# Optimization experiments

Measured on AMD Instinct MI355X. Metric: run time of the kernel, lower is better.

Reference implementation:

```python
import jax, jax.numpy as jnp
import numpy as np

B, T, D, H = 64, 512, 512, 1024


def setup_inputs() -> dict:
    key = jax.random.key(0)
    k1, k2, k3 = jax.random.split(key, 3)
    x = jax.random.normal(k1, (B, T, D), dtype=jnp.float32)
    W = jax.random.normal(k2, (D, 4 * H), dtype=jnp.float32) * 0.02  # input kernel
    U = jax.random.normal(k3, (H, 4 * H), dtype=jnp.float32) * 0.02  # recurrent kernel
    b = jnp.zeros((4 * H,), dtype=jnp.float32)
    return {"x": x, "W": W, "U": U, "b": b}


def reference(x, W, U, b):
    # Keras LSTM, gate order [i, f, c(g), o], sigmoid recurrent activation, tanh activation.
    # return_sequences=False, return_state=True -> pred == h_T; output = concat([h_T, h_T, c_T]).
    batch = x.shape[0]
    hidden = U.shape[0]

    def step(carry, xt):
        h, c = carry
        z = xt @ W + h @ U + b  # [B, 4H]
        i, f, g, o = jnp.split(z, 4, axis=-1)
        i = jax.nn.sigmoid(i)
        f = jax.nn.sigmoid(f)
        o = jax.nn.sigmoid(o)
        c_new = f * c + i * jnp.tanh(g)
        h_new = o * jnp.tanh(c_new)
        return (h_new, c_new), None

    h0 = jnp.zeros((batch, hidden), dtype=x.dtype)
    c0 = jnp.zeros((batch, hidden), dtype=x.dtype)
    xs = jnp.swapaxes(x, 0, 1)  # [T, B, D]
    (hT, cT), _ = jax.lax.scan(step, (h0, c0), xs)
    return jnp.concatenate([hT, hT, cT], axis=-1)  # [B, 3H]
```

## Files before the change

kernel.cpp:

```cpp
#include <hip/hip_runtime.h>
#include <stdint.h>

typedef unsigned short u16;

#define T_STEPS 512
#define BATCH   64
#define DIN     512
#define HID     1024
#define G4      4096
#define NBLK    128
#define NH      8
#define NC      32
#define THREADS 512

#define U_LD    1032
#define W_LD    520

#define SM_BYTES 99328
#define WT_OFF   66048

#define XB_BYTES ((size_t)T_STEPS * BATCH * DIN * 2)
#define HB_OFF   XB_BYTES
#define HB_BYTES (2u * 2u * 128 * 32 * 8 * 2)
#define FLG_OFF  (HB_OFF + HB_BYTES)
#define FLG_BYTES (2 * 128 * 4 * 16)
#define WS_NEED  (FLG_OFF + FLG_BYTES)

typedef float f32x16 __attribute__((ext_vector_type(16)));
typedef short bf16x8 __attribute__((ext_vector_type(8)));
typedef unsigned uint32x4 __attribute__((ext_vector_type(4)));

__device__ __forceinline__ u16 f2bf(float f) {
  unsigned u = __float_as_uint(f);
  u += 0x7fffu + ((u >> 16) & 1u);
  return (u16)(u >> 16);
}
__device__ __forceinline__ float sigm(float x) {
  return __builtin_amdgcn_rcpf(1.f + __expf(-x));
}
__device__ __forceinline__ float fast_tanh(float x) {
  return 1.f - 2.f * __builtin_amdgcn_rcpf(__expf(2.f * x) + 1.f);
}

__device__ __forceinline__ uint32x4 load16_sc(uint64_t addr) {
  uint32x4 d;
  asm volatile("global_load_dwordx4 %0, %1, off sc0 sc1" : "=v"(d) : "v"(addr));
  return d;
}
__device__ __forceinline__ uint32x4 load16_plain(uint64_t addr) {
  uint32x4 d;
  asm volatile("global_load_dwordx4 %0, %1, off" : "=v"(d) : "v"(addr));
  return d;
}
__device__ __forceinline__ unsigned load4_sc(uint64_t addr) {
  unsigned d;
  asm volatile("global_load_dword %0, %1, off sc0 sc1" : "=v"(d) : "v"(addr));
  return d;
}
__device__ __forceinline__ void store16_sc(uint64_t addr, uint32x4 v) {
  asm volatile("global_store_dwordx4 %0, %1, off sc0 sc1" :: "v"(addr), "v"(v) : "memory");
}
__device__ __forceinline__ void store4_sc(uint64_t addr, unsigned v) {
  asm volatile("global_store_dword %0, %1, off sc0 sc1" :: "v"(addr), "v"(v) : "memory");
}
#define WAITV(n) asm volatile("s_waitcnt vmcnt(" #n ")" ::: "memory")
#define SBAR()   __builtin_amdgcn_sched_barrier(0)

__global__ void cvt_x(const float* __restrict__ x, u16* __restrict__ xb) {
  int i = blockIdx.x * 256 + threadIdx.x;
  int dblk = i & 63;
  int rest = i >> 6;
  int b = rest & 63;
  int t = rest >> 6;
  const float4* s = reinterpret_cast<const float4*>(x + ((size_t)(b * T_STEPS + t)) * DIN + dblk * 8);
  float4 f0 = s[0], f1 = s[1];
  uint4 o;
  o.x = (unsigned)f2bf(f0.x) | ((unsigned)f2bf(f0.y) << 16);
  o.y = (unsigned)f2bf(f0.z) | ((unsigned)f2bf(f0.w) << 16);
  o.z = (unsigned)f2bf(f1.x) | ((unsigned)f2bf(f1.y) << 16);
  o.w = (unsigned)f2bf(f1.z) | ((unsigned)f2bf(f1.w) << 16);
  *reinterpret_cast<uint4*>(xb + ((size_t)(t * BATCH + b)) * DIN + dblk * 8) = o;
}

__launch_bounds__(THREADS)
__global__ void lstm_kernel(const float* __restrict__ W, const float* __restrict__ U,
                            const float* __restrict__ bias, const u16* __restrict__ xb,
                            char* __restrict__ ws, float* __restrict__ out) {
  __shared__ __align__(16) char smraw[SM_BYTES];
  u16* Ut = (u16*)smraw;
  u16* Wt = (u16*)(smraw + WT_OFF);
  float (*zp)[32][36] = (float(*)[32][36])smraw;

  const int tid = threadIdx.x;
  const int bid = blockIdx.x;
  const int j0 = bid * NH;

  for (int idx = tid; idx < NC * HID; idx += THREADS) {
    int c = idx & (NC - 1);
    int k = idx >> 5;
    int gcol = ((c & 3) << 10) + j0 + (c >> 2);
    Ut[c * U_LD + k] = f2bf(U[(size_t)k * G4 + gcol]);
  }
  for (int idx = tid; idx < NC * DIN; idx += THREADS) {
    int c = idx & (NC - 1);
    int k = idx >> 5;
    int gcol = ((c & 3) << 10) + j0 + (c >> 2);
    Wt[c * W_LD + k] = f2bf(W[(size_t)k * G4 + gcol]);
  }
  __syncthreads();

  const int l  = tid & 63;
  const int wv = tid >> 6;
  const int cl = l & 31;
  const int q  = l >> 5;

  bf16x8 ubf[8], wbf[4];
  {
    const u16* ub = Ut + cl * U_LD + wv * 128 + q * 8;
#pragma unroll
    for (int s = 0; s < 8; ++s) ubf[s] = *(const bf16x8*)(ub + s * 16);
    const u16* wb = Wt + cl * W_LD + wv * 64 + q * 8;
#pragma unroll
    for (int s = 0; s < 4; ++s) wbf[s] = *(const bf16x8*)(wb + s * 16);
  }
  __syncthreads();

  const int pb = tid >> 3;
  const int pu = tid & 7;
  const float bi  = bias[j0 + pu];
  const float bf_ = bias[1024 + j0 + pu];
  const float bg  = bias[2048 + j0 + pu];
  const float bo  = bias[3072 + j0 + pu];
  float cA = 0.f, cB = 0.f;
  int alive = 1;

  const uint64_t hbase = (uint64_t)ws + HB_OFF;
  const uint64_t fbase = (uint64_t)ws + FLG_OFF;
  const uint64_t xb64  = (uint64_t)xb;

  uint32x4 hA[8], xA[4], hB[8], xB[4];

  {
    const uint64_t hbp = hbase + (uint64_t)cl * 16;
#pragma unroll
    for (int s = 0; s < 8; ++s) hA[s] = load16_sc(hbp + (uint64_t)((wv * 16 + 2 * s + q) * 32) * 16);
    const uint64_t xap = xb64 + ((uint64_t)cl * 512 + (uint64_t)(wv * 64 + q * 8)) * 2;
#pragma unroll
    for (int s = 0; s < 4; ++s) xA[s] = load16_plain(xap + (uint64_t)s * 32);
  }

#define HMFMA(BUF, S) acc = __builtin_amdgcn_mfma_f32_32x32x16_bf16( \
    __builtin_bit_cast(bf16x8, BUF[S]), ubf[S], acc, 0, 0, 0)
#define XMFMA(BUF, S) acc = __builtin_amdgcn_mfma_f32_32x32x16_bf16( \
    __builtin_bit_cast(bf16x8, BUF[S]), wbf[S], acc, 0, 0, 0)

#define PHASE(CH, TT, HC, XC, HN, XN, CREG, OCH, OT) do {                        \
    WAITV(0); SBAR();             \
    f32x16 acc = {0.f,0.f,0.f,0.f,0.f,0.f,0.f,0.f,0.f,0.f,0.f,0.f,0.f,0.f,0.f,0.f}; \
    HMFMA(HC,0); HMFMA(HC,1); HMFMA(HC,2); HMFMA(HC,3);                          \
    HMFMA(HC,4); HMFMA(HC,5); HMFMA(HC,6); HMFMA(HC,7);                          \
    XMFMA(XC,0); XMFMA(XC,1); XMFMA(XC,2); XMFMA(XC,3);                          \
    _Pragma("unroll")                                                            \
    for (int r = 0; r < 16; ++r) {                                               \
      int rl = (r & 3) + 8 * (r >> 2) + 4 * q;                                   \
      zp[wv][rl][cl] = acc[r];                                                   \
    }                                                                            \
    __syncthreads();                                   \
    if (tid < 256) {                                                             \
      float zi = bi, zf = bf_, zg = bg, zo = bo;                                 \
      _Pragma("unroll")                                                          \
      for (int k2 = 0; k2 < 8; ++k2) {                                           \
        float4 v = *(const float4*)&zp[k2][pb][pu * 4];                          \
        zi += v.x; zf += v.y; zg += v.z; zo += v.w;                              \
      }                                                                          \
      float ig = sigm(zi), fg = sigm(zf), og = sigm(zo);                         \
      float gg = fast_tanh(zg);                                                  \
      CREG = fg * CREG + ig * gg;                                                \
      float h = og * fast_tanh(CREG);                                            \
      unsigned hval = (unsigned)f2bf(h);                                         \
      unsigned other = __shfl_xor(hval, 1);                                      \
      unsigned pair32 = (l & 1) ? ((other & 0xffffu) | (hval << 16))             \
                                : ((hval & 0xffffu) | (other << 16));            \
      int base_ = l & ~7;                                                        \
      uint32x4 hv;                                                               \
      hv[0] = __shfl(pair32, base_);     hv[1] = __shfl(pair32, base_ + 2);      \
      hv[2] = __shfl(pair32, base_ + 4); hv[3] = __shfl(pair32, base_ + 6);      \
      if ((l & 7) == 0)                                                          \
        store16_sc(hbase + (uint64_t)(CH) * 131072 +                             \
                   (uint64_t)(((TT) + 1) & 1) * 65536 + (uint64_t)bid * 512 +    \
                   (uint64_t)(wv * 8 + (l >> 3)) * 16, hv);                      \
      if ((TT) == T_STEPS - 1) {                                                 \
        float* orow = out + (size_t)((CH) * 32 + pb) * 3072 + j0 + pu;           \
        orow[0] = h; orow[1024] = h; orow[2048] = CREG;                          \
      }                                                                          \
      WAITV(0);                        \
      if (l == 0)                                                                \
        store4_sc(fbase + (uint64_t)(CH) * 8192 + (uint64_t)bid * 64 +           \
                  (uint64_t)wv * 16, (unsigned)((TT) + 1));                      \
    }                                                                            \
    if (alive) {                      \
      const uint64_t fa = fbase + (uint64_t)(OCH) * 8192 +                       \
                          (uint64_t)(wv * 16 + (l >> 2)) * 64 +                  \
                          (uint64_t)(l & 3) * 16;                                \
      int spins = 0;                                                             \
      while (true) {                                                             \
        unsigned f = load4_sc(fa);                                               \
        WAITV(0);                                                                \
        if (__all(f >= (unsigned)(OT))) break;                                   \
        if (++spins > (1 << 22)) { alive = 0; break; }                           \
        __builtin_amdgcn_s_sleep(1);                                             \
      }                                                                          \
    }                                                                            \
    {                                 \
      const uint64_t hbp = hbase + (uint64_t)(OCH) * 131072 +                    \
                           (uint64_t)((OT) & 1) * 65536 + (uint64_t)cl * 16;     \
      _Pragma("unroll")                                                          \
      for (int s = 0; s < 8; ++s)                                                \
        HN[s] = load16_sc(hbp + (uint64_t)((wv * 16 + 2 * s + q) * 32) * 16);    \
      const int otx = ((OT) < T_STEPS) ? (OT) : 0;                               \
      const uint64_t xap = xb64 + ((uint64_t)(otx * 64 + (OCH) * 32 + cl) * 512  \
                                   + (uint64_t)(wv * 64 + q * 8)) * 2;           \
      _Pragma("unroll")                                                          \
      for (int s = 0; s < 4; ++s) XN[s] = load16_plain(xap + (uint64_t)s * 32);  \
    }                                                                            \
    __syncthreads();                              \
  } while (0)

  for (int t = 0; t < T_STEPS; ++t) {
    PHASE(0, t, hA, xA, hB, xB, cA, 1, t);
    PHASE(1, t, hB, xB, hA, xA, cB, 0, t + 1);
  }
#undef PHASE
#undef HMFMA
#undef XMFMA
}

extern "C" void kernel_launch(void* const* d_in, const int* in_sizes, int n_in,
                              void* d_out, int out_size, void* d_ws, size_t ws_size,
                              hipStream_t stream) {
  const float* x = (const float*)d_in[0];
  const float* W = (const float*)d_in[1];
  const float* U = (const float*)d_in[2];
  const float* b = (const float*)d_in[3];
  float* out = (float*)d_out;

  if (ws_size < WS_NEED) return;

  u16* xb = (u16*)d_ws;
  hipMemsetAsync((char*)d_ws + HB_OFF, 0, HB_BYTES + FLG_BYTES, stream);
  cvt_x<<<(T_STEPS * BATCH * DIN / 8 + 255) / 256, 256, 0, stream>>>(x, xb);
  lstm_kernel<<<NBLK, THREADS, 0, stream>>>(W, U, b, xb, (char*)d_ws, out);
}
```

Measured before the change: 2.644 ms.

## Replace flag-based inter-block sync with timestamp-tagged hidden-state words

The separate flag array and its spin-wait are removed. Each bf16 hidden value is now packed into a 32-bit word together with a 16-bit step tag, so consumers speculatively load the next h bundle and check the tags, re-polling only when some are stale. This cuts the store-wait-flag-store round trip and the dependent load after the flag poll from the critical path of every recurrent step. In exchange the h buffer doubles in size and needs extra unpacking ALU work. Launch bounds also gain a minimum-blocks hint of 2.

```diff
diff --git a/kernel.cpp b/kernel.cpp
--- a/kernel.cpp
+++ b/kernel.cpp
@@ -21,10 +21,10 @@
 
 #define XB_BYTES ((size_t)T_STEPS * BATCH * DIN * 2)
 #define HB_OFF   XB_BYTES
-#define HB_BYTES (2u * 2u * 128 * 32 * 8 * 2)
-#define FLG_OFF  (HB_OFF + HB_BYTES)
-#define FLG_BYTES (2 * 128 * 4 * 16)
-#define WS_NEED  (FLG_OFF + FLG_BYTES)
+#define HB_PAR   131072
+#define HB_CH    (2 * HB_PAR)
+#define HB_BYTES (2u * HB_CH)
+#define WS_NEED  (HB_OFF + HB_BYTES)
 
 typedef float f32x16 __attribute__((ext_vector_type(16)));
 typedef short bf16x8 __attribute__((ext_vector_type(8)));
@@ -52,16 +52,8 @@
   asm volatile("global_load_dwordx4 %0, %1, off" : "=v"(d) : "v"(addr));
   return d;
 }
-__device__ __forceinline__ unsigned load4_sc(uint64_t addr) {
-  unsigned d;
-  asm volatile("global_load_dword %0, %1, off sc0 sc1" : "=v"(d) : "v"(addr));
-  return d;
-}
 __device__ __forceinline__ void store16_sc(uint64_t addr, uint32x4 v) {
   asm volatile("global_store_dwordx4 %0, %1, off sc0 sc1" :: "v"(addr), "v"(v) : "memory");
-}
-__device__ __forceinline__ void store4_sc(uint64_t addr, unsigned v) {
-  asm volatile("global_store_dword %0, %1, off sc0 sc1" :: "v"(addr), "v"(v) : "memory");
 }
 #define WAITV(n) asm volatile("s_waitcnt vmcnt(" #n ")" ::: "memory")
 #define SBAR()   __builtin_amdgcn_sched_barrier(0)
@@ -82,7 +74,7 @@
   *reinterpret_cast<uint4*>(xb + ((size_t)(t * BATCH + b)) * DIN + dblk * 8) = o;
 }
 
-__launch_bounds__(THREADS)
+__launch_bounds__(THREADS, 2)
 __global__ void lstm_kernel(const float* __restrict__ W, const float* __restrict__ U,
                             const float* __restrict__ bias, const u16* __restrict__ xb,
                             char* __restrict__ ws, float* __restrict__ out) {
@@ -135,36 +127,80 @@
   int alive = 1;
 
   const uint64_t hbase = (uint64_t)ws + HB_OFF;
-  const uint64_t fbase = (uint64_t)ws + FLG_OFF;
   const uint64_t xb64  = (uint64_t)xb;
-
-  uint32x4 hA[8], xA[4], hB[8], xB[4];
-
-  {
-    const uint64_t hbp = hbase + (uint64_t)cl * 16;
-#pragma unroll
-    for (int s = 0; s < 8; ++s) hA[s] = load16_sc(hbp + (uint64_t)((wv * 16 + 2 * s + q) * 32) * 16);
-    const uint64_t xap = xb64 + ((uint64_t)cl * 512 + (uint64_t)(wv * 64 + q * 8)) * 2;
-#pragma unroll
-    for (int s = 0; s < 4; ++s) xA[s] = load16_plain(xap + (uint64_t)s * 32);
-  }
-
-#define HMFMA(BUF, S) acc = __builtin_amdgcn_mfma_f32_32x32x16_bf16( \
-    __builtin_bit_cast(bf16x8, BUF[S]), ubf[S], acc, 0, 0, 0)
-#define XMFMA(BUF, S) acc = __builtin_amdgcn_mfma_f32_32x32x16_bf16( \
-    __builtin_bit_cast(bf16x8, BUF[S]), wbf[S], acc, 0, 0, 0)
-
-#define PHASE(CH, TT, HC, XC, HN, XN, CREG, OCH, OT) do {                        \
-    WAITV(0); SBAR();             \
+  const uint64_t hlane = (uint64_t)(wv * 16 + q) * 1024 + (uint64_t)cl * 32;
+  const uint64_t puboff = (uint64_t)bid * 1024 + (uint64_t)(tid >> 3) * 32 +
+                          (uint64_t)((l >> 2) & 1) * 16;
+
+  uint32x4 hbuf[16], xr[4];
+
+#define ISSUE_BUNDLE(NCH, NT) do {                                               \
+    const uint64_t hb_ = hbase + (uint64_t)(NCH) * HB_CH +                       \
+                         (uint64_t)((NT) & 1) * HB_PAR + hlane;                  \
+    _Pragma("unroll")                                                            \
+    for (int s_ = 0; s_ < 8; ++s_) {                                             \
+      hbuf[2 * s_]     = load16_sc(hb_ + (uint64_t)s_ * 2048);                   \
+      hbuf[2 * s_ + 1] = load16_sc(hb_ + (uint64_t)s_ * 2048 + 16);              \
+    }                                                                            \
+    const uint64_t xa_ = xb64 + (((uint64_t)(NT) * 64 + (NCH) * 32 + cl) * 512   \
+                                 + (uint64_t)(wv * 64 + q * 8)) * 2;             \
+    _Pragma("unroll")                                                            \
+    for (int s_ = 0; s_ < 4; ++s_) xr[s_] = load16_plain(xa_ + (uint64_t)s_ * 32); \
+  } while (0)
+
+#define PHASE(CH, TT, CREG, NCH, NT) do {                                        \
+    WAITV(0); SBAR();           \
+    const unsigned etag_ = (unsigned)(TT);                                       \
+    unsigned bad_ = 0;                                                           \
+    _Pragma("unroll")                                                            \
+    for (int s_ = 0; s_ < 16; ++s_) {                                            \
+      _Pragma("unroll")                                                          \
+      for (int e_ = 0; e_ < 4; ++e_) bad_ |= (hbuf[s_][e_] ^ etag_) & 0xffffu;   \
+    }                                                                            \
+    if (!__all(bad_ == 0)) {           \
+      int spins_ = 0;                                                            \
+      while (alive) {                                                            \
+        __builtin_amdgcn_s_sleep(2);                                             \
+        const uint64_t hb_ = hbase + (uint64_t)(CH) * HB_CH +                    \
+                             (uint64_t)((TT) & 1) * HB_PAR + hlane;              \
+        _Pragma("unroll")                                                        \
+        for (int s_ = 0; s_ < 8; ++s_) {                                         \
+          hbuf[2 * s_]     = load16_sc(hb_ + (uint64_t)s_ * 2048);               \
+          hbuf[2 * s_ + 1] = load16_sc(hb_ + (uint64_t)s_ * 2048 + 16);          \
+        }                                                                        \
+        WAITV(0); SBAR();                                                        \
+        bad_ = 0;                                                                \
+        _Pragma("unroll")                                                        \
+        for (int s_ = 0; s_ < 16; ++s_) {                                        \
+          _Pragma("unroll")                                                      \
+          for (int e_ = 0; e_ < 4; ++e_) bad_ |= (hbuf[s_][e_] ^ etag_) & 0xffffu; \
+        }                                                                        \
+        if (__all(bad_ == 0)) break;                                             \
+        if (++spins_ > (1 << 18)) { alive = 0; break; }                          \
+      }                                                                          \
+    }                                                                            \
     f32x16 acc = {0.f,0.f,0.f,0.f,0.f,0.f,0.f,0.f,0.f,0.f,0.f,0.f,0.f,0.f,0.f,0.f}; \
-    HMFMA(HC,0); HMFMA(HC,1); HMFMA(HC,2); HMFMA(HC,3);                          \
-    HMFMA(HC,4); HMFMA(HC,5); HMFMA(HC,6); HMFMA(HC,7);                          \
-    XMFMA(XC,0); XMFMA(XC,1); XMFMA(XC,2); XMFMA(XC,3);                          \
-    _Pragma("unroll")                                                            \
-    for (int r = 0; r < 16; ++r) {                                               \
-      int rl = (r & 3) + 8 * (r >> 2) + 4 * q;                                   \
-      zp[wv][rl][cl] = acc[r];                                                   \
-    }                                                                            \
+    _Pragma("unroll")                                                            \
+    for (int s_ = 0; s_ < 8; ++s_) {          \
+      uint32x4 d0_ = hbuf[2 * s_], d1_ = hbuf[2 * s_ + 1];                       \
+      uint32x4 pk_;                                                              \
+      pk_[0] = (d0_[0] >> 16) | (d0_[1] & 0xffff0000u);                          \
+      pk_[1] = (d0_[2] >> 16) | (d0_[3] & 0xffff0000u);                          \
+      pk_[2] = (d1_[0] >> 16) | (d1_[1] & 0xffff0000u);                          \
+      pk_[3] = (d1_[2] >> 16) | (d1_[3] & 0xffff0000u);                          \
+      acc = __builtin_amdgcn_mfma_f32_32x32x16_bf16(                             \
+          __builtin_bit_cast(bf16x8, pk_), ubf[s_], acc, 0, 0, 0);               \
+    }                                                                            \
+    _Pragma("unroll")                                                            \
+    for (int s_ = 0; s_ < 4; ++s_)                                      \
+      acc = __builtin_amdgcn_mfma_f32_32x32x16_bf16(                             \
+          __builtin_bit_cast(bf16x8, xr[s_]), wbf[s_], acc, 0, 0, 0);            \
+    _Pragma("unroll")                                                            \
+    for (int r_ = 0; r_ < 16; ++r_) {      \
+      int rl_ = (r_ & 3) + 8 * (r_ >> 2) + 4 * q;                                \
+      zp[wv][rl_][cl] = acc[r_];                                                 \
+    }                                                                            \
+    ISSUE_BUNDLE(NCH, NT);       \
     __syncthreads();                                   \
     if (tid < 256) {                                                             \
       float zi = bi, zf = bf_, zg = bg, zo = bo;                                 \
@@ -177,62 +213,31 @@
       float gg = fast_tanh(zg);                                                  \
       CREG = fg * CREG + ig * gg;                                                \
       float h = og * fast_tanh(CREG);                                            \
-      unsigned hval = (unsigned)f2bf(h);                                         \
-      unsigned other = __shfl_xor(hval, 1);                                      \
-      unsigned pair32 = (l & 1) ? ((other & 0xffffu) | (hval << 16))             \
-                                : ((hval & 0xffffu) | (other << 16));            \
-      int base_ = l & ~7;                                                        \
+      unsigned hval = ((unsigned)f2bf(h) << 16) | ((unsigned)((TT) + 1) & 0xffffu); \
+      int base_ = l & ~3;                                                        \
       uint32x4 hv;                                                               \
-      hv[0] = __shfl(pair32, base_);     hv[1] = __shfl(pair32, base_ + 2);      \
-      hv[2] = __shfl(pair32, base_ + 4); hv[3] = __shfl(pair32, base_ + 6);      \
-      if ((l & 7) == 0)                                                          \
-        store16_sc(hbase + (uint64_t)(CH) * 131072 +                             \
-                   (uint64_t)(((TT) + 1) & 1) * 65536 + (uint64_t)bid * 512 +    \
-                   (uint64_t)(wv * 8 + (l >> 3)) * 16, hv);                      \
+      hv[0] = __shfl(hval, base_);     hv[1] = __shfl(hval, base_ + 1);          \
+      hv[2] = __shfl(hval, base_ + 2); hv[3] = __shfl(hval, base_ + 3);          \
+      if ((l & 3) == 0)                                                          \
+        store16_sc(hbase + (uint64_t)(CH) * HB_CH +                              \
+                   (uint64_t)(((TT) + 1) & 1) * HB_PAR + puboff, hv);            \
       if ((TT) == T_STEPS - 1) {                                                 \
         float* orow = out + (size_t)((CH) * 32 + pb) * 3072 + j0 + pu;           \
         orow[0] = h; orow[1024] = h; orow[2048] = CREG;                          \
       }                                                                          \
-      WAITV(0);                        \
-      if (l == 0)                                                                \
-        store4_sc(fbase + (uint64_t)(CH) * 8192 + (uint64_t)bid * 64 +           \
-                  (uint64_t)wv * 16, (unsigned)((TT) + 1));                      \
-    }                                                                            \
-    if (alive) {                      \
-      const uint64_t fa = fbase + (uint64_t)(OCH) * 8192 +                       \
-                          (uint64_t)(wv * 16 + (l >> 2)) * 64 +                  \
-                          (uint64_t)(l & 3) * 16;                                \
-      int spins = 0;                                                             \
-      while (true) {                                                             \
-        unsigned f = load4_sc(fa);                                               \
-        WAITV(0);                                                                \
-        if (__all(f >= (unsigned)(OT))) break;                                   \
-        if (++spins > (1 << 22)) { alive = 0; break; }                           \
-        __builtin_amdgcn_s_sleep(1);                                             \
-      }                                                                          \
-    }                                                                            \
-    {                                 \
-      const uint64_t hbp = hbase + (uint64_t)(OCH) * 131072 +                    \
-                           (uint64_t)((OT) & 1) * 65536 + (uint64_t)cl * 16;     \
-      _Pragma("unroll")                                                          \
-      for (int s = 0; s < 8; ++s)                                                \
-        HN[s] = load16_sc(hbp + (uint64_t)((wv * 16 + 2 * s + q) * 32) * 16);    \
-      const int otx = ((OT) < T_STEPS) ? (OT) : 0;                               \
-      const uint64_t xap = xb64 + ((uint64_t)(otx * 64 + (OCH) * 32 + cl) * 512  \
-                                   + (uint64_t)(wv * 64 + q * 8)) * 2;           \
-      _Pragma("unroll")                                                          \
-      for (int s = 0; s < 4; ++s) XN[s] = load16_plain(xap + (uint64_t)s * 32);  \
-    }                                                                            \
-    __syncthreads();                              \
+    }                                                                            \
+    __syncthreads();           \
   } while (0)
 
+  ISSUE_BUNDLE(0, 0);
+
   for (int t = 0; t < T_STEPS; ++t) {
-    PHASE(0, t, hA, xA, hB, xB, cA, 1, t);
-    PHASE(1, t, hB, xB, hA, xA, cB, 0, t + 1);
+    const int tn = (t + 1 < T_STEPS) ? (t + 1) : (T_STEPS - 1);
+    PHASE(0, t, cA, 1, t);
+    PHASE(1, t, cB, 0, tn);
   }
 #undef PHASE
-#undef HMFMA
-#undef XMFMA
+#undef ISSUE_BUNDLE
 }
 
 extern "C" void kernel_launch(void* const* d_in, const int* in_sizes, int n_in,
@@ -247,7 +252,7 @@
   if (ws_size < WS_NEED) return;
 
   u16* xb = (u16*)d_ws;
-  hipMemsetAsync((char*)d_ws + HB_OFF, 0, HB_BYTES + FLG_BYTES, stream);
+  hipMemsetAsync((char*)d_ws + HB_OFF, 0, HB_BYTES, stream);
   cvt_x<<<(T_STEPS * BATCH * DIN / 8 + 255) / 256, 256, 0, stream>>>(x, xb);
   lstm_kernel<<<NBLK, THREADS, 0, stream>>>(W, U, b, xb, (char*)d_ws, out);
 }
```

Result: slower. 3.338 ms (+26.3%).

## Halve persistent LSTM blocks to 64, each owning 16 hidden units

Applied to the files above, without the earlier changes.

The persistent recurrent kernel now runs 64 blocks instead of 128, and each block holds 64 gate columns (16 hidden units) of U and W in registers as two MFMA accumulators. All 512 threads now compute the gate nonlinearities. The per-wave completion flags are replaced by one flag per block, published after a block barrier, and polled by a single wave of 64 lanes. The aim is to cut cross-block synchronisation traffic and polling per step and to put more MFMA work in each block. In exchange it doubles register pressure for the weight fragments, adds one extra barrier per phase, and drops the double-buffered h/x registers, so the next loads are no longer overlapped with the barrier.

```diff
diff --git a/kernel.cpp b/kernel.cpp
--- a/kernel.cpp
+++ b/kernel.cpp
@@ -8,22 +8,23 @@
 #define DIN     512
 #define HID     1024
 #define G4      4096
-#define NBLK    128
-#define NH      8
-#define NC      32
+#define NBLK    64
+#define NH      16
+#define NC      64
 #define THREADS 512
 
 #define U_LD    1032
 #define W_LD    520
 
-#define SM_BYTES 99328
-#define WT_OFF   66048
+#define SM_BYTES 69632
 
 #define XB_BYTES ((size_t)T_STEPS * BATCH * DIN * 2)
 #define HB_OFF   XB_BYTES
-#define HB_BYTES (2u * 2u * 128 * 32 * 8 * 2)
+#define HB_PAR   65536
+#define HB_CH    (2 * HB_PAR)
+#define HB_BYTES (2u * HB_CH)
 #define FLG_OFF  (HB_OFF + HB_BYTES)
-#define FLG_BYTES (2 * 128 * 4 * 16)
+#define FLG_BYTES (2 * 64 * 16)
 #define WS_NEED  (FLG_OFF + FLG_BYTES)
 
 typedef float f32x16 __attribute__((ext_vector_type(16)));
@@ -82,51 +83,59 @@
   *reinterpret_cast<uint4*>(xb + ((size_t)(t * BATCH + b)) * DIN + dblk * 8) = o;
 }
 
-__launch_bounds__(THREADS)
+__launch_bounds__(THREADS, 2)
 __global__ void lstm_kernel(const float* __restrict__ W, const float* __restrict__ U,
                             const float* __restrict__ bias, const u16* __restrict__ xb,
                             char* __restrict__ ws, float* __restrict__ out) {
   __shared__ __align__(16) char smraw[SM_BYTES];
-  u16* Ut = (u16*)smraw;
-  u16* Wt = (u16*)(smraw + WT_OFF);
-  float (*zp)[32][36] = (float(*)[32][36])smraw;
+  u16* stage = (u16*)smraw;
+  float (*zp)[32][68] = (float(*)[32][68])smraw;
 
   const int tid = threadIdx.x;
   const int bid = blockIdx.x;
   const int j0 = bid * NH;
-
-  for (int idx = tid; idx < NC * HID; idx += THREADS) {
-    int c = idx & (NC - 1);
-    int k = idx >> 5;
-    int gcol = ((c & 3) << 10) + j0 + (c >> 2);
-    Ut[c * U_LD + k] = f2bf(U[(size_t)k * G4 + gcol]);
-  }
-  for (int idx = tid; idx < NC * DIN; idx += THREADS) {
-    int c = idx & (NC - 1);
-    int k = idx >> 5;
-    int gcol = ((c & 3) << 10) + j0 + (c >> 2);
-    Wt[c * W_LD + k] = f2bf(W[(size_t)k * G4 + gcol]);
-  }
-  __syncthreads();
 
   const int l  = tid & 63;
   const int wv = tid >> 6;
   const int cl = l & 31;
   const int q  = l >> 5;
 
-  bf16x8 ubf[8], wbf[4];
-  {
-    const u16* ub = Ut + cl * U_LD + wv * 128 + q * 8;
-#pragma unroll
-    for (int s = 0; s < 8; ++s) ubf[s] = *(const bf16x8*)(ub + s * 16);
-    const u16* wb = Wt + cl * W_LD + wv * 64 + q * 8;
-#pragma unroll
-    for (int s = 0; s < 4; ++s) wbf[s] = *(const bf16x8*)(wb + s * 16);
+  bf16x8 ubf[2][8], wbf[2][4];
+#pragma unroll
+  for (int ph = 0; ph < 2; ++ph) {
+    for (int idx = tid; idx < 32 * HID; idx += THREADS) {
+      int cc = idx & 31, k = idx >> 5;
+      int c = ph * 32 + cc;
+      int gcol = ((c & 3) << 10) + j0 + (c >> 2);
+      stage[cc * U_LD + k] = f2bf(U[(size_t)k * G4 + gcol]);
+    }
+    __syncthreads();
+    {
+      const u16* ub = stage + cl * U_LD + wv * 128 + q * 8;
+#pragma unroll
+      for (int s = 0; s < 8; ++s) ubf[ph][s] = *(const bf16x8*)(ub + s * 16);
+    }
+    __syncthreads();
   }
-  __syncthreads();
-
-  const int pb = tid >> 3;
-  const int pu = tid & 7;
+#pragma unroll
+  for (int ph = 0; ph < 2; ++ph) {
+    for (int idx = tid; idx < 32 * DIN; idx += THREADS) {
+      int cc = idx & 31, k = idx >> 5;
+      int c = ph * 32 + cc;
+      int gcol = ((c & 3) << 10) + j0 + (c >> 2);
+      stage[cc * W_LD + k] = f2bf(W[(size_t)k * G4 + gcol]);
+    }
+    __syncthreads();
+    {
+      const u16* wb = stage + cl * W_LD + wv * 64 + q * 8;
+#pragma unroll
+      for (int s = 0; s < 4; ++s) wbf[ph][s] = *(const bf16x8*)(wb + s * 16);
+    }
+    __syncthreads();
+  }
+
+  const int pb = tid >> 4;
+  const int pu = tid & 15;
   const float bi  = bias[j0 + pu];
   const float bf_ = bias[1024 + j0 + pu];
   const float bg  = bias[2048 + j0 + pu];
@@ -137,36 +146,48 @@
   const uint64_t hbase = (uint64_t)ws + HB_OFF;
   const uint64_t fbase = (uint64_t)ws + FLG_OFF;
   const uint64_t xb64  = (uint64_t)xb;
-
-  uint32x4 hA[8], xA[4], hB[8], xB[4];
-
-  {
-    const uint64_t hbp = hbase + (uint64_t)cl * 16;
-#pragma unroll
-    for (int s = 0; s < 8; ++s) hA[s] = load16_sc(hbp + (uint64_t)((wv * 16 + 2 * s + q) * 32) * 16);
-    const uint64_t xap = xb64 + ((uint64_t)cl * 512 + (uint64_t)(wv * 64 + q * 8)) * 2;
-#pragma unroll
-    for (int s = 0; s < 4; ++s) xA[s] = load16_plain(xap + (uint64_t)s * 32);
-  }
-
-#define HMFMA(BUF, S) acc = __builtin_amdgcn_mfma_f32_32x32x16_bf16( \
-    __builtin_bit_cast(bf16x8, BUF[S]), ubf[S], acc, 0, 0, 0)
-#define XMFMA(BUF, S) acc = __builtin_amdgcn_mfma_f32_32x32x16_bf16( \
-    __builtin_bit_cast(bf16x8, BUF[S]), wbf[S], acc, 0, 0, 0)
-
-#define PHASE(CH, TT, HC, XC, HN, XN, CREG, OCH, OT) do {                        \
-    WAITV(0); SBAR();             \
-    f32x16 acc = {0.f,0.f,0.f,0.f,0.f,0.f,0.f,0.f,0.f,0.f,0.f,0.f,0.f,0.f,0.f,0.f}; \
-    HMFMA(HC,0); HMFMA(HC,1); HMFMA(HC,2); HMFMA(HC,3);                          \
-    HMFMA(HC,4); HMFMA(HC,5); HMFMA(HC,6); HMFMA(HC,7);                          \
-    XMFMA(XC,0); XMFMA(XC,1); XMFMA(XC,2); XMFMA(XC,3);                          \
-    _Pragma("unroll")                                                            \
-    for (int r = 0; r < 16; ++r) {                                               \
-      int rl = (r & 3) + 8 * (r >> 2) + 4 * q;                                   \
-      zp[wv][rl][cl] = acc[r];                                                   \
+  const uint64_t hlane = (uint64_t)wv * 8192 + (uint64_t)cl * 32 + (uint64_t)q * 16;
+  const uint64_t puboff = (uint64_t)bid * 1024 + (uint64_t)(tid >> 4) * 32 +
+                          (uint64_t)((l >> 3) & 1) * 16;
+  const uint64_t pollo = (uint64_t)l * 16;
+
+  uint32x4 hbuf[8], xr[4];
+
+#define ISSUE_BUNDLE(NCH, NT) do {                                               \
+    const uint64_t hb_ = hbase + (uint64_t)(NCH) * HB_CH +                       \
+                         (uint64_t)((NT) & 1) * HB_PAR + hlane;                  \
+    _Pragma("unroll")                                                            \
+    for (int s_ = 0; s_ < 8; ++s_) hbuf[s_] = load16_sc(hb_ + (uint64_t)s_ * 1024); \
+    const uint64_t xa_ = xb64 + (((uint64_t)(NT) * 64 + (NCH) * 32 + cl) * 512   \
+                                 + (uint64_t)(wv * 64 + q * 8)) * 2;             \
+    _Pragma("unroll")                                                            \
+    for (int s_ = 0; s_ < 4; ++s_) xr[s_] = load16_plain(xa_ + (uint64_t)s_ * 32); \
+  } while (0)
+
+#define PHASE(CH, TT, CREG, OCH, OT) do {                                        \
+    WAITV(0); SBAR();         \
+    f32x16 acc0 = {0.f,0.f,0.f,0.f,0.f,0.f,0.f,0.f,0.f,0.f,0.f,0.f,0.f,0.f,0.f,0.f}; \
+    f32x16 acc1 = {0.f,0.f,0.f,0.f,0.f,0.f,0.f,0.f,0.f,0.f,0.f,0.f,0.f,0.f,0.f,0.f}; \
+    _Pragma("unroll")                                                            \
+    for (int s_ = 0; s_ < 8; ++s_) {         \
+      bf16x8 a_ = __builtin_bit_cast(bf16x8, hbuf[s_]);                          \
+      acc0 = __builtin_amdgcn_mfma_f32_32x32x16_bf16(a_, ubf[0][s_], acc0, 0, 0, 0); \
+      acc1 = __builtin_amdgcn_mfma_f32_32x32x16_bf16(a_, ubf[1][s_], acc1, 0, 0, 0); \
+    }                                                                            \
+    _Pragma("unroll")                                                            \
+    for (int s_ = 0; s_ < 4; ++s_) {                                    \
+      bf16x8 a_ = __builtin_bit_cast(bf16x8, xr[s_]);                            \
+      acc0 = __builtin_amdgcn_mfma_f32_32x32x16_bf16(a_, wbf[0][s_], acc0, 0, 0, 0); \
+      acc1 = __builtin_amdgcn_mfma_f32_32x32x16_bf16(a_, wbf[1][s_], acc1, 0, 0, 0); \
+    }                                                                            \
+    _Pragma("unroll")                                                            \
+    for (int r_ = 0; r_ < 16; ++r_) {      \
+      int rl_ = (r_ & 3) + 8 * (r_ >> 2) + 4 * q;                                \
+      zp[wv][rl_][cl]      = acc0[r_];                                           \
+      zp[wv][rl_][32 + cl] = acc1[r_];                                           \
     }                                                                            \
     __syncthreads();                                   \
-    if (tid < 256) {                                                             \
+    {                                                                            \
       float zi = bi, zf = bf_, zg = bg, zo = bo;                                 \
       _Pragma("unroll")                                                          \
       for (int k2 = 0; k2 < 8; ++k2) {                                           \
@@ -186,53 +207,41 @@
       hv[0] = __shfl(pair32, base_);     hv[1] = __shfl(pair32, base_ + 2);      \
       hv[2] = __shfl(pair32, base_ + 4); hv[3] = __shfl(pair32, base_ + 6);      \
       if ((l & 7) == 0)                                                          \
-        store16_sc(hbase + (uint64_t)(CH) * 131072 +                             \
-                   (uint64_t)(((TT) + 1) & 1) * 65536 + (uint64_t)bid * 512 +    \
-                   (uint64_t)(wv * 8 + (l >> 3)) * 16, hv);                      \
+        store16_sc(hbase + (uint64_t)(CH) * HB_CH +                              \
+                   (uint64_t)(((TT) + 1) & 1) * HB_PAR + puboff, hv);            \
       if ((TT) == T_STEPS - 1) {                                                 \
         float* orow = out + (size_t)((CH) * 32 + pb) * 3072 + j0 + pu;           \
         orow[0] = h; orow[1024] = h; orow[2048] = CREG;                          \
       }                                                                          \
-      WAITV(0);                        \
-      if (l == 0)                                                                \
-        store4_sc(fbase + (uint64_t)(CH) * 8192 + (uint64_t)bid * 64 +           \
-                  (uint64_t)wv * 16, (unsigned)((TT) + 1));                      \
-    }                                                                            \
-    if (alive) {                      \
-      const uint64_t fa = fbase + (uint64_t)(OCH) * 8192 +                       \
-                          (uint64_t)(wv * 16 + (l >> 2)) * 64 +                  \
-                          (uint64_t)(l & 3) * 16;                                \
+    }                                                                            \
+    WAITV(0);                      \
+    __syncthreads();          \
+    if (tid == 0)                                          \
+      store4_sc(fbase + (uint64_t)(CH) * 1024 + (uint64_t)bid * 16,              \
+                (unsigned)((TT) + 1));                                           \
+    if (alive) {           \
+      const uint64_t fa = fbase + (uint64_t)(OCH) * 1024 + pollo;                \
       int spins = 0;                                                             \
       while (true) {                                                             \
         unsigned f = load4_sc(fa);                                               \
         WAITV(0);                                                                \
         if (__all(f >= (unsigned)(OT))) break;                                   \
-        if (++spins > (1 << 22)) { alive = 0; break; }                           \
+        if (++spins > (1 << 20)) { alive = 0; break; }                           \
         __builtin_amdgcn_s_sleep(1);                                             \
       }                                                                          \
     }                                                                            \
-    {                                 \
-      const uint64_t hbp = hbase + (uint64_t)(OCH) * 131072 +                    \
-                           (uint64_t)((OT) & 1) * 65536 + (uint64_t)cl * 16;     \
-      _Pragma("unroll")                                                          \
-      for (int s = 0; s < 8; ++s)                                                \
-        HN[s] = load16_sc(hbp + (uint64_t)((wv * 16 + 2 * s + q) * 32) * 16);    \
-      const int otx = ((OT) < T_STEPS) ? (OT) : 0;                               \
-      const uint64_t xap = xb64 + ((uint64_t)(otx * 64 + (OCH) * 32 + cl) * 512  \
-                                   + (uint64_t)(wv * 64 + q * 8)) * 2;           \
-      _Pragma("unroll")                                                          \
-      for (int s = 0; s < 4; ++s) XN[s] = load16_plain(xap + (uint64_t)s * 32);  \
-    }                                                                            \
-    __syncthreads();                              \
+    ISSUE_BUNDLE(OCH, OT);                    \
   } while (0)
 
+  ISSUE_BUNDLE(0, 0);
+
   for (int t = 0; t < T_STEPS; ++t) {
-    PHASE(0, t, hA, xA, hB, xB, cA, 1, t);
-    PHASE(1, t, hB, xB, hA, xA, cB, 0, t + 1);
+    const int tn = (t + 1 < T_STEPS) ? (t + 1) : (T_STEPS - 1);
+    PHASE(0, t, cA, 1, t);
+    PHASE(1, t, cB, 0, tn);
   }
 #undef PHASE
-#undef HMFMA
-#undef XMFMA
+#undef ISSUE_BUNDLE
 }
 
 extern "C" void kernel_launch(void* const* d_in, const int* in_sizes, int n_in,
```

Result: slower. 3.613 ms (+36.6%).

## Pipeline four 16-row batch chunks with 128-slot h ring and speculative flag polling

Applied to the files above, without the earlier changes.

Splits the batch into four 16-row chunks processed in a rotating pipeline, switching from 32x32 to 16x16x32 bf16 MFMAs with each wave covering two N-tiles over a K-split of four. Hidden states go to a 128-slot ring buffer in workspace, which lets prefetch use plain loads and be issued before the reduction. Flags drop to one dword per block, and a speculatively preloaded flag vector is checked before any spin loop. The intent is to overlap inter-block synchronization latency with computation on other chunks and to shrink barrier and flag traffic. The risks are more phases per step, correctness depending on ring-slot reuse and weaker cache coherence for the plain loads, and a shorter spin timeout.

```diff
diff --git a/kernel.cpp b/kernel.cpp
--- a/kernel.cpp
+++ b/kernel.cpp
@@ -21,12 +21,14 @@
 
 #define XB_BYTES ((size_t)T_STEPS * BATCH * DIN * 2)
 #define HB_OFF   XB_BYTES
-#define HB_BYTES (2u * 2u * 128 * 32 * 8 * 2)
+#define SLAB     131072
+#define NSLOT    128
+#define HB_BYTES ((size_t)NSLOT * SLAB)
 #define FLG_OFF  (HB_OFF + HB_BYTES)
-#define FLG_BYTES (2 * 128 * 4 * 16)
+#define FLG_BYTES 4096
 #define WS_NEED  (FLG_OFF + FLG_BYTES)
 
-typedef float f32x16 __attribute__((ext_vector_type(16)));
+typedef float f32x4 __attribute__((ext_vector_type(4)));
 typedef short bf16x8 __attribute__((ext_vector_type(8)));
 typedef unsigned uint32x4 __attribute__((ext_vector_type(4)));
 
@@ -42,19 +44,14 @@
   return 1.f - 2.f * __builtin_amdgcn_rcpf(__expf(2.f * x) + 1.f);
 }
 
-__device__ __forceinline__ uint32x4 load16_sc(uint64_t addr) {
-  uint32x4 d;
-  asm volatile("global_load_dwordx4 %0, %1, off sc0 sc1" : "=v"(d) : "v"(addr));
-  return d;
-}
 __device__ __forceinline__ uint32x4 load16_plain(uint64_t addr) {
   uint32x4 d;
   asm volatile("global_load_dwordx4 %0, %1, off" : "=v"(d) : "v"(addr));
   return d;
 }
-__device__ __forceinline__ unsigned load4_sc(uint64_t addr) {
-  unsigned d;
-  asm volatile("global_load_dword %0, %1, off sc0 sc1" : "=v"(d) : "v"(addr));
+__device__ __forceinline__ uint32x4 load16_sc(uint64_t addr) {
+  uint32x4 d;
+  asm volatile("global_load_dwordx4 %0, %1, off sc0 sc1" : "=v"(d) : "v"(addr));
   return d;
 }
 __device__ __forceinline__ void store16_sc(uint64_t addr, uint32x4 v) {
@@ -89,7 +86,7 @@
   __shared__ __align__(16) char smraw[SM_BYTES];
   u16* Ut = (u16*)smraw;
   u16* Wt = (u16*)(smraw + WT_OFF);
-  float (*zp)[32][36] = (float(*)[32][36])smraw;
+  float* zp = (float*)smraw;
 
   const int tid = threadIdx.x;
   const int bid = blockIdx.x;
@@ -98,30 +95,33 @@
   for (int idx = tid; idx < NC * HID; idx += THREADS) {
     int c = idx & (NC - 1);
     int k = idx >> 5;
-    int gcol = ((c & 3) << 10) + j0 + (c >> 2);
+    int gcol = ((c >> 3) << 10) + j0 + (c & 7);
     Ut[c * U_LD + k] = f2bf(U[(size_t)k * G4 + gcol]);
   }
   for (int idx = tid; idx < NC * DIN; idx += THREADS) {
     int c = idx & (NC - 1);
     int k = idx >> 5;
-    int gcol = ((c & 3) << 10) + j0 + (c >> 2);
+    int gcol = ((c >> 3) << 10) + j0 + (c & 7);
     Wt[c * W_LD + k] = f2bf(W[(size_t)k * G4 + gcol]);
   }
   __syncthreads();
 
-  const int l  = tid & 63;
-  const int wv = tid >> 6;
-  const int cl = l & 31;
-  const int q  = l >> 5;
-
-  bf16x8 ubf[8], wbf[4];
-  {
-    const u16* ub = Ut + cl * U_LD + wv * 128 + q * 8;
+  const int l   = tid & 63;
+  const int wv  = tid >> 6;
+  const int ks  = wv >> 1;
+  const int nt  = wv & 1;
+  const int r16 = l & 15;
+  const int q4  = l >> 4;
+
+  bf16x8 ubf[2][8], wbf[2][4];
 #pragma unroll
-    for (int s = 0; s < 8; ++s) ubf[s] = *(const bf16x8*)(ub + s * 16);
-    const u16* wb = Wt + cl * W_LD + wv * 64 + q * 8;
+  for (int n_ = 0; n_ < 2; ++n_) {
+    const u16* ub = Ut + (n_ * 16 + r16) * U_LD + ks * 256 + q4 * 8;
 #pragma unroll
-    for (int s = 0; s < 4; ++s) wbf[s] = *(const bf16x8*)(wb + s * 16);
+    for (int s = 0; s < 8; ++s) ubf[n_][s] = *(const bf16x8*)(ub + s * 32);
+    const u16* wb = Wt + (n_ * 16 + r16) * W_LD + ks * 128 + q4 * 8;
+#pragma unroll
+    for (int s = 0; s < 4; ++s) wbf[n_][s] = *(const bf16x8*)(wb + s * 32);
   }
   __syncthreads();
 
@@ -131,47 +131,83 @@
   const float bf_ = bias[1024 + j0 + pu];
   const float bg  = bias[2048 + j0 + pu];
   const float bo  = bias[3072 + j0 + pu];
-  float cA = 0.f, cB = 0.f;
+  float c0 = 0.f, c1 = 0.f, c2 = 0.f, c3 = 0.f;
   int alive = 1;
 
-  const uint64_t hbase = (uint64_t)ws + HB_OFF;
+  const uint64_t hbB   = (uint64_t)ws + HB_OFF;
   const uint64_t fbase = (uint64_t)ws + FLG_OFF;
   const uint64_t xb64  = (uint64_t)xb;
-
-  uint32x4 hA[8], xA[4], hB[8], xB[4];
-
-  {
-    const uint64_t hbp = hbase + (uint64_t)cl * 16;
-#pragma unroll
-    for (int s = 0; s < 8; ++s) hA[s] = load16_sc(hbp + (uint64_t)((wv * 16 + 2 * s + q) * 32) * 16);
-    const uint64_t xap = xb64 + ((uint64_t)cl * 512 + (uint64_t)(wv * 64 + q * 8)) * 2;
-#pragma unroll
-    for (int s = 0; s < 4; ++s) xA[s] = load16_plain(xap + (uint64_t)s * 32);
-  }
-
-#define HMFMA(BUF, S) acc = __builtin_amdgcn_mfma_f32_32x32x16_bf16( \
-    __builtin_bit_cast(bf16x8, BUF[S]), ubf[S], acc, 0, 0, 0)
-#define XMFMA(BUF, S) acc = __builtin_amdgcn_mfma_f32_32x32x16_bf16( \
-    __builtin_bit_cast(bf16x8, BUF[S]), wbf[S], acc, 0, 0, 0)
-
-#define PHASE(CH, TT, HC, XC, HN, XN, CREG, OCH, OT) do {                        \
-    WAITV(0); SBAR();             \
-    f32x16 acc = {0.f,0.f,0.f,0.f,0.f,0.f,0.f,0.f,0.f,0.f,0.f,0.f,0.f,0.f,0.f,0.f}; \
-    HMFMA(HC,0); HMFMA(HC,1); HMFMA(HC,2); HMFMA(HC,3);                          \
-    HMFMA(HC,4); HMFMA(HC,5); HMFMA(HC,6); HMFMA(HC,7);                          \
-    XMFMA(XC,0); XMFMA(XC,1); XMFMA(XC,2); XMFMA(XC,3);                          \
-    _Pragma("unroll")                                                            \
-    for (int r = 0; r < 16; ++r) {                                               \
-      int rl = (r & 3) + 8 * (r >> 2) + 4 * q;                                   \
-      zp[wv][rl][cl] = acc[r];                                                   \
-    }                                                                            \
-    __syncthreads();                                   \
-    if (tid < 256) {                                                             \
+  const uint64_t fwoff = (uint64_t)ks * 128 + (uint64_t)(l & 7) * 16;
+
+  uint32x4 hbuf[8], xr[4];
+  uint32x4 specf;
+
+#define ISSUE_PF(PFC, PFT) do {                                                  \
+    const uint64_t slab_ = hbB + (uint64_t)((PFT) & (NSLOT - 1)) * SLAB;         \
+    _Pragma("unroll")                                                            \
+    for (int s_ = 0; s_ < 8; ++s_)                                               \
+      hbuf[s_] = load16_plain(slab_ + (uint64_t)((ks * 32 + s_ * 4 + q4) * 1024) \
+                              + (uint64_t)((PFC) * 16 + r16) * 16);              \
+    const int xt_ = ((PFT) < T_STEPS) ? (PFT) : (T_STEPS - 1);                   \
+    const uint64_t xa_ = xb64 + (((uint64_t)xt_ * 64 + (PFC) * 16 + r16) * 512   \
+                                 + (uint64_t)(ks * 128 + q4 * 8)) * 2;           \
+    _Pragma("unroll")                                                            \
+    for (int s_ = 0; s_ < 4; ++s_) xr[s_] = load16_plain(xa_ + (uint64_t)s_ * 64); \
+  } while (0)
+
+#define PHASE(CH, TT, CREG, PFC, PFT, SPC, FLC, FLV) do {                        \
+    WAITV(0); SBAR();      \
+    {         \
+      const unsigned need_ = (unsigned)(PFT);                                    \
+      bool ok_ = (specf[0] >= need_) & (specf[1] >= need_) &                     \
+                 (specf[2] >= need_) & (specf[3] >= need_);                      \
+      if (!__all(ok_)) {                        \
+        const uint64_t fa_ = fbase + (uint64_t)(PFC) * 512 + fwoff;              \
+        int spins_ = 0;                                                          \
+        while (alive) {                                                          \
+          uint32x4 f_ = load16_sc(fa_);                                          \
+          WAITV(0);                                                              \
+          bool o2_ = (f_[0] >= need_) & (f_[1] >= need_) &                       \
+                     (f_[2] >= need_) & (f_[3] >= need_);                        \
+          if (__all(o2_)) break;                                                 \
+          if (++spins_ > (1 << 18)) { alive = 0; break; }                        \
+          __builtin_amdgcn_s_sleep(1);                                           \
+        }                                                                        \
+      }                                                                          \
+    }                                                                            \
+                   \
+    specf = load16_sc(fbase + (uint64_t)(SPC) * 512 + fwoff);                    \
+          \
+    f32x4 acc0 = {0.f, 0.f, 0.f, 0.f};                                           \
+    f32x4 acc1 = {0.f, 0.f, 0.f, 0.f};                                           \
+    _Pragma("unroll")                                                            \
+    for (int s_ = 0; s_ < 8; ++s_) {                                             \
+      bf16x8 a_ = __builtin_bit_cast(bf16x8, hbuf[s_]);                          \
+      acc0 = __builtin_amdgcn_mfma_f32_16x16x32_bf16(a_, ubf[0][s_], acc0, 0, 0, 0); \
+      acc1 = __builtin_amdgcn_mfma_f32_16x16x32_bf16(a_, ubf[1][s_], acc1, 0, 0, 0); \
+    }                                                                            \
+    _Pragma("unroll")                                                            \
+    for (int s_ = 0; s_ < 4; ++s_) {                                             \
+      bf16x8 a_ = __builtin_bit_cast(bf16x8, xr[s_]);                            \
+      acc0 = __builtin_amdgcn_mfma_f32_16x16x32_bf16(a_, wbf[0][s_], acc0, 0, 0, 0); \
+      acc1 = __builtin_amdgcn_mfma_f32_16x16x32_bf16(a_, wbf[1][s_], acc1, 0, 0, 0); \
+    }                                                                            \
+    ISSUE_PF(PFC, PFT);            \
+    _Pragma("unroll")                                                            \
+    for (int r_ = 0; r_ < 4; ++r_) {            \
+      zp[ks * 528 + (q4 * 4 + r_) * 33 + r16]      = acc0[r_];                   \
+      zp[ks * 528 + (q4 * 4 + r_) * 33 + 16 + r16] = acc1[r_];                   \
+    }                                                                            \
+    __syncthreads();               \
+    if (tid == 0)         \
+      store4_sc(fbase + (uint64_t)(FLC) * 512 + (uint64_t)bid * 4,               \
+                (unsigned)(FLV));                                                \
+    if (tid < 128) {                               \
       float zi = bi, zf = bf_, zg = bg, zo = bo;                                 \
       _Pragma("unroll")                                                          \
-      for (int k2 = 0; k2 < 8; ++k2) {                                           \
-        float4 v = *(const float4*)&zp[k2][pb][pu * 4];                          \
-        zi += v.x; zf += v.y; zg += v.z; zo += v.w;                              \
+      for (int k2 = 0; k2 < 4; ++k2) {                                           \
+        const float* zr = zp + k2 * 528 + pb * 33;                               \
+        zi += zr[pu]; zf += zr[pu + 8]; zg += zr[pu + 16]; zo += zr[pu + 24];    \
       }                                                                          \
       float ig = sigm(zi), fg = sigm(zf), og = sigm(zo);                         \
       float gg = fast_tanh(zg);                                                  \
@@ -181,58 +217,32 @@
       unsigned other = __shfl_xor(hval, 1);                                      \
       unsigned pair32 = (l & 1) ? ((other & 0xffffu) | (hval << 16))             \
                                 : ((hval & 0xffffu) | (other << 16));            \
-      int base_ = l & ~7;                                                        \
+      int bl_ = l & ~7;                                                          \
       uint32x4 hv;                                                               \
-      hv[0] = __shfl(pair32, base_);     hv[1] = __shfl(pair32, base_ + 2);      \
-      hv[2] = __shfl(pair32, base_ + 4); hv[3] = __shfl(pair32, base_ + 6);      \
-      if ((l & 7) == 0)                                                          \
-        store16_sc(hbase + (uint64_t)(CH) * 131072 +                             \
-                   (uint64_t)(((TT) + 1) & 1) * 65536 + (uint64_t)bid * 512 +    \
-                   (uint64_t)(wv * 8 + (l >> 3)) * 16, hv);                      \
+      hv[0] = __shfl(pair32, bl_);     hv[1] = __shfl(pair32, bl_ + 2);          \
+      hv[2] = __shfl(pair32, bl_ + 4); hv[3] = __shfl(pair32, bl_ + 6);          \
+      if ((l & 7) == 0)                  \
+        store16_sc(hbB + (uint64_t)(((TT) + 1) & (NSLOT - 1)) * SLAB +           \
+                   (uint64_t)bid * 1024 + (uint64_t)((CH) * 16 + pb) * 16, hv);  \
       if ((TT) == T_STEPS - 1) {                                                 \
-        float* orow = out + (size_t)((CH) * 32 + pb) * 3072 + j0 + pu;           \
+        float* orow = out + (size_t)((CH) * 16 + pb) * 3072 + j0 + pu;           \
         orow[0] = h; orow[1024] = h; orow[2048] = CREG;                          \
       }                                                                          \
-      WAITV(0);                        \
-      if (l == 0)                                                                \
-        store4_sc(fbase + (uint64_t)(CH) * 8192 + (uint64_t)bid * 64 +           \
-                  (uint64_t)wv * 16, (unsigned)((TT) + 1));                      \
-    }                                                                            \
-    if (alive) {                      \
-      const uint64_t fa = fbase + (uint64_t)(OCH) * 8192 +                       \
-                          (uint64_t)(wv * 16 + (l >> 2)) * 64 +                  \
-                          (uint64_t)(l & 3) * 16;                                \
-      int spins = 0;                                                             \
-      while (true) {                                                             \
-        unsigned f = load4_sc(fa);                                               \
-        WAITV(0);                                                                \
-        if (__all(f >= (unsigned)(OT))) break;                                   \
-        if (++spins > (1 << 22)) { alive = 0; break; }                           \
-        __builtin_amdgcn_s_sleep(1);                                             \
-      }                                                                          \
-    }                                                                            \
-    {                                 \
-      const uint64_t hbp = hbase + (uint64_t)(OCH) * 131072 +                    \
-                           (uint64_t)((OT) & 1) * 65536 + (uint64_t)cl * 16;     \
-      _Pragma("unroll")                                                          \
-      for (int s = 0; s < 8; ++s)                                                \
-        HN[s] = load16_sc(hbp + (uint64_t)((wv * 16 + 2 * s + q) * 32) * 16);    \
-      const int otx = ((OT) < T_STEPS) ? (OT) : 0;                               \
-      const uint64_t xap = xb64 + ((uint64_t)(otx * 64 + (OCH) * 32 + cl) * 512  \
-                                   + (uint64_t)(wv * 64 + q * 8)) * 2;           \
-      _Pragma("unroll")                                                          \
-      for (int s = 0; s < 4; ++s) XN[s] = load16_plain(xap + (uint64_t)s * 32);  \
-    }                                                                            \
-    __syncthreads();                              \
+    }                                                                            \
+    __syncthreads();           \
   } while (0)
 
+  ISSUE_PF(0, 0);
+  specf = load16_sc(fbase + 512 + fwoff);
+
   for (int t = 0; t < T_STEPS; ++t) {
-    PHASE(0, t, hA, xA, hB, xB, cA, 1, t);
-    PHASE(1, t, hB, xB, hA, xA, cB, 0, t + 1);
+    PHASE(0,  t, c0,  1,  t,     2,  3,  t    );
+    PHASE(1,  t, c1,  2,  t,     3,  0,  t + 1);
+    PHASE(2,  t, c2,  3,  t,     0,  1,  t + 1);
+    PHASE(3,  t, c3,  0,  t + 1, 1,  2,  t + 1);
   }
 #undef PHASE
-#undef HMFMA
-#undef XMFMA
+#undef ISSUE_PF
 }
 
 extern "C" void kernel_launch(void* const* d_in, const int* in_sizes, int n_in,
@@ -247,7 +257,9 @@
   if (ws_size < WS_NEED) return;
 
   u16* xb = (u16*)d_ws;
-  hipMemsetAsync((char*)d_ws + HB_OFF, 0, HB_BYTES + FLG_BYTES, stream);
+
+  hipMemsetAsync((char*)d_ws + HB_OFF, 0, SLAB, stream);
+  hipMemsetAsync((char*)d_ws + FLG_OFF, 0, FLG_BYTES, stream);
   cvt_x<<<(T_STEPS * BATCH * DIN / 8 + 255) / 256, 256, 0, stream>>>(x, xb);
   lstm_kernel<<<NBLK, THREADS, 0, stream>>>(W, U, b, xb, (char*)d_ws, out);
 }
```

New measurement: 3.837 ms. 1.45x slower.
